# Performance work log

Hardware: AMD Instinct MI355X
Metric: run time of the kernel (lower is better)

The kernel has to match this reference:

```python
import jax, jax.numpy as jnp
import numpy as np

N_NODES = 100000
N_EDGES = 1600000
HIDDEN = 512
LOWER = 128
NUM_RELS = 6


def setup_inputs() -> dict:
    key = jax.random.key(0)
    ks = jax.random.split(key, 16)
    glorot = lambda k, shape: jax.random.normal(k, shape, jnp.float32) * (2.0 / (shape[-2] + shape[-1])) ** 0.5
    return {
        "h_origin": jax.random.normal(ks[0], (N_NODES, HIDDEN), jnp.float32),
        "edge_src": jax.random.randint(ks[1], (N_EDGES,), 0, N_NODES, jnp.int32),
        "edge_dst": jax.random.randint(ks[2], (N_EDGES,), 0, N_NODES, jnp.int32),
        "edge_type": jax.random.randint(ks[3], (N_EDGES,), 0, NUM_RELS, jnp.int32),
        "W_lower": glorot(ks[4], (HIDDEN, LOWER)),
        "b_lower": jnp.zeros((LOWER,), jnp.float32),
        "W1": glorot(ks[5], (NUM_RELS, LOWER, LOWER)),
        "b1": jnp.zeros((LOWER,), jnp.float32),
        "W2": glorot(ks[6], (NUM_RELS, LOWER, LOWER)),
        "b2": jnp.zeros((LOWER,), jnp.float32),
        "W3": glorot(ks[7], (NUM_RELS, LOWER, LOWER)),
        "b3": jnp.zeros((LOWER,), jnp.float32),
        "W_upper": glorot(ks[8], (LOWER, HIDDEN)),
        "b_upper": jnp.zeros((HIDDEN,), jnp.float32),
        "W_skip": glorot(ks[9], (HIDDEN, HIDDEN)),
        "b_skip": jnp.zeros((HIDDEN,), jnp.float32),
    }


def _ngcn_layer(h, W, b, edge_src, edge_dst, edge_type, n_nodes):
    # R-GCN layer: msg_e = h[src_e] @ W[rel_e]; h'_v = relu(sum_{e->v} msg_e + b)
    # Equivalent grouped form: transform all nodes by all relations (dense GEMMs),
    # then gather per-edge by (rel, src) -- same math as per-edge bmm.
    t = jnp.einsum("nd,rde->rne", h, W)          # [R, N, out]
    msg = t[edge_type, edge_src]                   # [E, out] gather
    agg = jax.ops.segment_sum(msg, edge_dst, num_segments=n_nodes)  # [N, out]
    return jax.nn.relu(agg + b)


def reference(h_origin, edge_src, edge_dst, edge_type,
              W_lower, b_lower, W1, b1, W2, b2, W3, b3,
              W_upper, b_upper, W_skip, b_skip):
    n_nodes = h_origin.shape[0]
    # lower: Linear + ReLU (hidden -> lower)
    h = jax.nn.relu(h_origin @ W_lower + b_lower)
    # three NGCN (R-GCN) layers, num_rels = 6
    h = _ngcn_layer(h, W1, b1, edge_src, edge_dst, edge_type, n_nodes)
    h = _ngcn_layer(h, W2, b2, edge_src, edge_dst, edge_type, n_nodes)
    h = _ngcn_layer(h, W3, b3, edge_src, edge_dst, edge_type, n_nodes)
    # upper(h) + skipper(origin): bg.ndata['h'] = upper(h) + skipper(origin_ndata)
    out = jax.nn.relu(h @ W_upper + b_upper) + jax.nn.relu(h_origin @ W_skip + b_skip)
    return out
```

## Files before the change

kernel.cpp:

```cpp
#include <hip/hip_runtime.h>
#include <hip/hip_bf16.h>

#define NN 100000
#define NE 1600000
#define HID 512
#define LOW 128
#define NR  6
#define NBINS (NN * NR)

typedef short  bf16x8 __attribute__((ext_vector_type(8)));
typedef float  f32x4  __attribute__((ext_vector_type(4)));

__device__ __forceinline__ unsigned short f2bf(float x) {
    __hip_bfloat16 h = __float2bfloat16(x);
    return __builtin_bit_cast(unsigned short, h);
}
__device__ __forceinline__ float bf2f(unsigned short u) {
    return __builtin_bit_cast(float, (unsigned int)u << 16);
}

__device__ __forceinline__ void stage_tile(const unsigned short* __restrict__ G,
                                           int r0, int k0, int Kstride, int Rmax,
                                           char* lds_base, int tid)
{
    #pragma unroll
    for (int is = 0; is < 4; ++is) {
        int L   = is * 4096 + tid * 16;
        int row = L >> 7;
        int c   = ((L >> 4) & 7) ^ (row & 7);
        int gr  = r0 + row;
        gr = (gr < Rmax) ? gr : (Rmax - 1);
        const char* src = (const char*)G + ((size_t)gr * Kstride + k0) * 2 + c * 16;
        __builtin_amdgcn_global_load_lds(
            (const __attribute__((address_space(1))) void*)src,
            (__attribute__((address_space(3))) void*)(lds_base + is * 4096 + (tid & 192) * 16),
            16, 0, 0);
    }
}

__device__ __forceinline__ bf16x8 lds_frag(const char* lds_base, int row, int clog)
{
    return *(const bf16x8*)(lds_base + row * 128 + ((clog ^ (row & 7)) << 4));
}

__global__ __launch_bounds__(256, 2)
void gemm_bf16(const unsigned short* __restrict__ A,
               const unsigned short* __restrict__ Bt,
               const float* __restrict__ bias,
               unsigned short* __restrict__ C,
               int M, int N, int K)
{
    __shared__ __align__(16) char lA[16384];
    __shared__ __align__(16) char lB[16384];

    const int tid  = threadIdx.x;
    const int lane = tid & 63;
    const int wid  = tid >> 6;
    const int wm   = wid >> 1;
    const int wn   = wid & 1;
    const int m0   = blockIdx.y * 128;
    const int n0   = blockIdx.x * 128;

    f32x4 acc[4][4] = {};

    for (int k0 = 0; k0 < K; k0 += 64) {
        stage_tile(A,  m0, k0, K, M, lA, tid);
        stage_tile(Bt, n0, k0, K, N, lB, tid);
        __syncthreads();
        #pragma unroll
        for (int kk = 0; kk < 2; ++kk) {
            const int clog = kk * 4 + (lane >> 4);
            bf16x8 af[4], bfr[4];
            #pragma unroll
            for (int i = 0; i < 4; ++i)
                af[i] = lds_frag(lA, wm * 64 + i * 16 + (lane & 15), clog);
            #pragma unroll
            for (int j = 0; j < 4; ++j)
                bfr[j] = lds_frag(lB, wn * 64 + j * 16 + (lane & 15), clog);
            #pragma unroll
            for (int i = 0; i < 4; ++i)
                #pragma unroll
                for (int j = 0; j < 4; ++j)
                    acc[i][j] = __builtin_amdgcn_mfma_f32_16x16x32_bf16(
                        af[i], bfr[j], acc[i][j], 0, 0, 0);
        }
        __syncthreads();
    }

    const int col_l = lane & 15;
    const int rgrp  = lane >> 4;
    #pragma unroll
    for (int i = 0; i < 4; ++i) {
        #pragma unroll
        for (int j = 0; j < 4; ++j) {
            int col  = n0 + wn * 64 + j * 16 + col_l;
            float bv = bias[col];
            #pragma unroll
            for (int r = 0; r < 4; ++r) {
                int row = m0 + wm * 64 + i * 16 + rgrp * 4 + r;
                if (row < M)
                    C[(size_t)row * N + col] = f2bf(fmaxf(acc[i][j][r] + bv, 0.f));
            }
        }
    }
}

__global__ __launch_bounds__(256, 2)
void gemm_out_fused(const unsigned short* __restrict__ h,
                    const unsigned short* __restrict__ Wut,
                    const float* __restrict__ bu,
                    const unsigned short* __restrict__ hob,
                    const unsigned short* __restrict__ Wst,
                    const float* __restrict__ bs,
                    float* __restrict__ out, int M)
{
    __shared__ __align__(16) char lA[16384];
    __shared__ __align__(16) char lB[16384];

    const int tid  = threadIdx.x;
    const int lane = tid & 63;
    const int wid  = tid >> 6;
    const int wm   = wid >> 1;
    const int wn   = wid & 1;

    const int nwg  = gridDim.x;
    const int cpx  = nwg >> 3;
    const int idx  = (blockIdx.x & 7) * cpx + (blockIdx.x >> 3);
    const int m0   = (idx >> 2) * 128;
    const int n0   = (idx & 3) * 128;

    f32x4 acc1[4][4] = {};
    f32x4 acc2[4][4] = {};

    for (int k0 = 0; k0 < LOW; k0 += 64) {
        stage_tile(h,   m0, k0, LOW, M,   lA, tid);
        stage_tile(Wut, n0, k0, LOW, HID, lB, tid);
        __syncthreads();
        #pragma unroll
        for (int kk = 0; kk < 2; ++kk) {
            const int clog = kk * 4 + (lane >> 4);
            bf16x8 af[4], bfr[4];
            #pragma unroll
            for (int i = 0; i < 4; ++i)
                af[i] = lds_frag(lA, wm * 64 + i * 16 + (lane & 15), clog);
            #pragma unroll
            for (int j = 0; j < 4; ++j)
                bfr[j] = lds_frag(lB, wn * 64 + j * 16 + (lane & 15), clog);
            #pragma unroll
            for (int i = 0; i < 4; ++i)
                #pragma unroll
                for (int j = 0; j < 4; ++j)
                    acc1[i][j] = __builtin_amdgcn_mfma_f32_16x16x32_bf16(
                        af[i], bfr[j], acc1[i][j], 0, 0, 0);
        }
        __syncthreads();
    }
    for (int k0 = 0; k0 < HID; k0 += 64) {
        stage_tile(hob, m0, k0, HID, M,   lA, tid);
        stage_tile(Wst, n0, k0, HID, HID, lB, tid);
        __syncthreads();
        #pragma unroll
        for (int kk = 0; kk < 2; ++kk) {
            const int clog = kk * 4 + (lane >> 4);
            bf16x8 af[4], bfr[4];
            #pragma unroll
            for (int i = 0; i < 4; ++i)
                af[i] = lds_frag(lA, wm * 64 + i * 16 + (lane & 15), clog);
            #pragma unroll
            for (int j = 0; j < 4; ++j)
                bfr[j] = lds_frag(lB, wn * 64 + j * 16 + (lane & 15), clog);
            #pragma unroll
            for (int i = 0; i < 4; ++i)
                #pragma unroll
                for (int j = 0; j < 4; ++j)
                    acc2[i][j] = __builtin_amdgcn_mfma_f32_16x16x32_bf16(
                        af[i], bfr[j], acc2[i][j], 0, 0, 0);
        }
        __syncthreads();
    }

    const int col_l = lane & 15;
    const int rgrp  = lane >> 4;
    #pragma unroll
    for (int i = 0; i < 4; ++i) {
        #pragma unroll
        for (int j = 0; j < 4; ++j) {
            int col   = n0 + wn * 64 + j * 16 + col_l;
            float bv1 = bu[col], bv2 = bs[col];
            #pragma unroll
            for (int r = 0; r < 4; ++r) {
                int row = m0 + wm * 64 + i * 16 + rgrp * 4 + r;
                if (row < M)
                    out[(size_t)row * HID + col] =
                        fmaxf(acc1[i][j][r] + bv1, 0.f) + fmaxf(acc2[i][j][r] + bv2, 0.f);
            }
        }
    }
}

__global__ __launch_bounds__(256)
void conv_f32_bf16(const float4* __restrict__ in, ushort4* __restrict__ out, int n4)
{
    for (int i = blockIdx.x * 256 + threadIdx.x; i < n4; i += gridDim.x * 256) {
        float4 v = in[i];
        ushort4 o;
        o.x = f2bf(v.x); o.y = f2bf(v.y); o.z = f2bf(v.z); o.w = f2bf(v.w);
        out[i] = o;
    }
}

__global__ __launch_bounds__(256)
void transpose_all(const float* __restrict__ Wl_, const float* __restrict__ W1,
                   const float* __restrict__ W2, const float* __restrict__ W3,
                   const float* __restrict__ Wu, const float* __restrict__ Ws_,
                   unsigned short* __restrict__ wlt, unsigned short* __restrict__ w1t,
                   unsigned short* __restrict__ w2t, unsigned short* __restrict__ w3t,
                   unsigned short* __restrict__ wut, unsigned short* __restrict__ wst)
{
    int idx = blockIdx.x * 256 + threadIdx.x;
    const float* W;
    unsigned short* T;
    int R, local, cshift;
    if (idx < 65536)       { W = Wl_; T = wlt; R = 512; local = idx;          cshift = 7; }
    else if (idx < 163840) { W = W1;  T = w1t; R = 768; local = idx - 65536;  cshift = 7; }
    else if (idx < 262144) { W = W2;  T = w2t; R = 768; local = idx - 163840; cshift = 7; }
    else if (idx < 360448) { W = W3;  T = w3t; R = 768; local = idx - 262144; cshift = 7; }
    else if (idx < 425984) { W = Wu;  T = wut; R = 128; local = idx - 360448; cshift = 9; }
    else                   { W = Ws_; T = wst; R = 512; local = idx - 425984; cshift = 9; }
    int r = local >> cshift;
    int c = local & ((1 << cshift) - 1);
    T[(size_t)c * R + r] = f2bf(W[local]);
}

#define SCAN_VT 8
#define SCAN_BS 256
#define SCAN_CHUNK (SCAN_VT * SCAN_BS)
#define SCAN_NB ((NBINS + SCAN_CHUNK - 1) / SCAN_CHUNK)

__global__ __launch_bounds__(256)
void k_hist(const int* __restrict__ dst, const int* __restrict__ typ,
            int* __restrict__ deg, int E)
{
    int e = blockIdx.x * 256 + threadIdx.x;
    if (e < E) atomicAdd(&deg[dst[e] * NR + typ[e]], 1);
}

__global__ __launch_bounds__(SCAN_BS)
void k_scan_part(const int* __restrict__ deg, int* __restrict__ blocksum, int n)
{
    __shared__ int ps[SCAN_BS];
    const int t = threadIdx.x;
    const int lo = blockIdx.x * SCAN_CHUNK + t * SCAN_VT;
    int s = 0;
    #pragma unroll
    for (int k = 0; k < SCAN_VT; ++k) {
        int i = lo + k;
        if (i < n) s += deg[i];
    }
    ps[t] = s;
    __syncthreads();
    for (int off = SCAN_BS / 2; off > 0; off >>= 1) {
        if (t < off) ps[t] += ps[t + off];
        __syncthreads();
    }
    if (t == 0) blocksum[blockIdx.x] = ps[0];
}

__global__ __launch_bounds__(64)
void k_scan_mid(const int* __restrict__ blocksum, int* __restrict__ blockoff,
                int* __restrict__ rowstart, int nb, int n)
{
    if (threadIdx.x == 0) {
        int run = 0;
        for (int i = 0; i < nb; ++i) { blockoff[i] = run; run += blocksum[i]; }
        rowstart[n] = run;
    }
}

__global__ __launch_bounds__(SCAN_BS)
void k_scan_final(const int* __restrict__ deg, const int* __restrict__ blockoff,
                  int* __restrict__ rowstart, int* __restrict__ cursor, int n)
{
    __shared__ int ps[SCAN_BS];
    const int t = threadIdx.x;
    const int lo = blockIdx.x * SCAN_CHUNK + t * SCAN_VT;
    int local[SCAN_VT];
    int s = 0;
    #pragma unroll
    for (int k = 0; k < SCAN_VT; ++k) {
        int i = lo + k;
        int v = (i < n) ? deg[i] : 0;
        local[k] = v;
        s += v;
    }
    ps[t] = s;
    __syncthreads();
    for (int off = 1; off < SCAN_BS; off <<= 1) {
        int v = (t >= off) ? ps[t - off] : 0;
        __syncthreads();
        ps[t] += v;
        __syncthreads();
    }
    int run = blockoff[blockIdx.x] + ((t > 0) ? ps[t - 1] : 0);
    #pragma unroll
    for (int k = 0; k < SCAN_VT; ++k) {
        int i = lo + k;
        if (i < n) {
            rowstart[i] = run;
            cursor[i]   = run;
            run += local[k];
        }
    }
}

__global__ __launch_bounds__(256)
void k_fill(const int* __restrict__ src, const int* __restrict__ dst,
            const int* __restrict__ typ, int* __restrict__ cursor,
            int* __restrict__ list, int E)
{
    int e = blockIdx.x * 256 + threadIdx.x;
    if (e < E) {
        int pos = atomicAdd(&cursor[dst[e] * NR + typ[e]], 1);
        list[pos] = src[e];
    }
}

__global__ __launch_bounds__(256)
void gather_agg(const unsigned short* __restrict__ h,
                const int* __restrict__ rowstart,
                const int* __restrict__ list,
                unsigned short* __restrict__ S)
{
    const int v = (blockIdx.x * 256 + threadIdx.x) >> 5;
    if (v >= NN) return;
    const int lane = threadIdx.x & 31;
    const ushort4* hp = (const ushort4*)h;

    const int b0 = rowstart[v * NR + 0];
    const int b1 = rowstart[v * NR + 1];
    const int b2 = rowstart[v * NR + 2];
    const int b3 = rowstart[v * NR + 3];
    const int b4 = rowstart[v * NR + 4];
    const int b5 = rowstart[v * NR + 5];
    const int b6 = rowstart[v * NR + 6];
    const int n0 = b1 - b0, n1 = b2 - b1, n2 = b3 - b2;
    const int n3 = b4 - b3, n4 = b5 - b4, n5 = b6 - b5;
    const int kmax = max(max(max(n0, n1), max(n2, n3)), max(n4, n5));

    float a0x=0.f,a0y=0.f,a0z=0.f,a0w=0.f, a1x=0.f,a1y=0.f,a1z=0.f,a1w=0.f;
    float a2x=0.f,a2y=0.f,a2z=0.f,a2w=0.f, a3x=0.f,a3y=0.f,a3z=0.f,a3w=0.f;
    float a4x=0.f,a4y=0.f,a4z=0.f,a4w=0.f, a5x=0.f,a5y=0.f,a5z=0.f,a5w=0.f;

    for (int k = 0; k < kmax; ++k) {
        int i0 = (k < n0) ? (b0 + k) : 0;
        int i1 = (k < n1) ? (b1 + k) : 0;
        int i2 = (k < n2) ? (b2 + k) : 0;
        int i3 = (k < n3) ? (b3 + k) : 0;
        int i4 = (k < n4) ? (b4 + k) : 0;
        int i5 = (k < n5) ? (b5 + k) : 0;
        int s0 = list[i0], s1 = list[i1], s2 = list[i2];
        int s3 = list[i3], s4 = list[i4], s5 = list[i5];
        ushort4 u0 = hp[(size_t)s0 * 32 + lane];
        ushort4 u1 = hp[(size_t)s1 * 32 + lane];
        ushort4 u2 = hp[(size_t)s2 * 32 + lane];
        ushort4 u3 = hp[(size_t)s3 * 32 + lane];
        ushort4 u4 = hp[(size_t)s4 * 32 + lane];
        ushort4 u5 = hp[(size_t)s5 * 32 + lane];
        if (k < n0) { a0x += bf2f(u0.x); a0y += bf2f(u0.y); a0z += bf2f(u0.z); a0w += bf2f(u0.w); }
        if (k < n1) { a1x += bf2f(u1.x); a1y += bf2f(u1.y); a1z += bf2f(u1.z); a1w += bf2f(u1.w); }
        if (k < n2) { a2x += bf2f(u2.x); a2y += bf2f(u2.y); a2z += bf2f(u2.z); a2w += bf2f(u2.w); }
        if (k < n3) { a3x += bf2f(u3.x); a3y += bf2f(u3.y); a3z += bf2f(u3.z); a3w += bf2f(u3.w); }
        if (k < n4) { a4x += bf2f(u4.x); a4y += bf2f(u4.y); a4z += bf2f(u4.z); a4w += bf2f(u4.w); }
        if (k < n5) { a5x += bf2f(u5.x); a5y += bf2f(u5.y); a5z += bf2f(u5.z); a5w += bf2f(u5.w); }
    }

    ushort4* o = (ushort4*)(S + (size_t)v * (NR * LOW));
    ushort4 w;
    w.x=f2bf(a0x); w.y=f2bf(a0y); w.z=f2bf(a0z); w.w=f2bf(a0w); o[0*32+lane]=w;
    w.x=f2bf(a1x); w.y=f2bf(a1y); w.z=f2bf(a1z); w.w=f2bf(a1w); o[1*32+lane]=w;
    w.x=f2bf(a2x); w.y=f2bf(a2y); w.z=f2bf(a2z); w.w=f2bf(a2w); o[2*32+lane]=w;
    w.x=f2bf(a3x); w.y=f2bf(a3y); w.z=f2bf(a3z); w.w=f2bf(a3w); o[3*32+lane]=w;
    w.x=f2bf(a4x); w.y=f2bf(a4y); w.z=f2bf(a4z); w.w=f2bf(a4w); o[4*32+lane]=w;
    w.x=f2bf(a5x); w.y=f2bf(a5y); w.z=f2bf(a5z); w.w=f2bf(a5w); o[5*32+lane]=w;
}

extern "C" void kernel_launch(void* const* d_in, const int* in_sizes, int n_in,
                              void* d_out, int out_size, void* d_ws, size_t ws_size,
                              hipStream_t stream)
{
    (void)in_sizes; (void)n_in; (void)out_size; (void)ws_size;

    const float* h_origin = (const float*)d_in[0];
    const int*   esrc     = (const int*)d_in[1];
    const int*   edst     = (const int*)d_in[2];
    const int*   etyp     = (const int*)d_in[3];
    const float* W_lower  = (const float*)d_in[4];
    const float* b_lower  = (const float*)d_in[5];
    const float* Wl[3]    = {(const float*)d_in[6], (const float*)d_in[8], (const float*)d_in[10]};
    const float* bl[3]    = {(const float*)d_in[7], (const float*)d_in[9], (const float*)d_in[11]};
    const float* W_upper  = (const float*)d_in[12];
    const float* b_upper  = (const float*)d_in[13];
    const float* W_skip   = (const float*)d_in[14];
    const float* b_skip   = (const float*)d_in[15];
    float*       out      = (float*)d_out;

    unsigned short* hob = (unsigned short*)d_ws;
    unsigned short* h   = hob + (size_t)NN * HID;
    unsigned short* S   = h + (size_t)NN * LOW;
    unsigned short* wlt = S + (size_t)NN * NR * LOW;
    unsigned short* w1t = wlt + (size_t)LOW * HID;
    unsigned short* w2t = w1t + (size_t)LOW * NR * LOW;
    unsigned short* w3t = w2t + (size_t)LOW * NR * LOW;
    unsigned short* wut = w3t + (size_t)LOW * NR * LOW;
    unsigned short* wst = wut + (size_t)HID * LOW;
    int* deg      = (int*)(wst + (size_t)HID * HID);
    int* rowstart = deg + NBINS;
    int* cursor   = rowstart + NBINS + 1;
    int* list     = cursor + NBINS;
    int* blocksum = list + NE;
    int* blockoff = blocksum + SCAN_NB;
    unsigned short* wtL[3] = {w1t, w2t, w3t};

    const unsigned eBlocks = (unsigned)((NE + 255) / 256);
    const unsigned mBlocks = (unsigned)((NN + 127) / 128);

    conv_f32_bf16<<<dim3(2048), dim3(256), 0, stream>>>(
        (const float4*)h_origin, (ushort4*)hob, NN * HID / 4);
    transpose_all<<<dim3(2688), dim3(256), 0, stream>>>(
        W_lower, Wl[0], Wl[1], Wl[2], W_upper, W_skip,
        wlt, w1t, w2t, w3t, wut, wst);

    hipMemsetAsync(deg, 0, NBINS * sizeof(int), stream);
    k_hist<<<dim3(eBlocks), dim3(256), 0, stream>>>(edst, etyp, deg, NE);
    k_scan_part<<<dim3(SCAN_NB), dim3(SCAN_BS), 0, stream>>>(deg, blocksum, NBINS);
    k_scan_mid<<<dim3(1), dim3(64), 0, stream>>>(blocksum, blockoff, rowstart, SCAN_NB, NBINS);
    k_scan_final<<<dim3(SCAN_NB), dim3(SCAN_BS), 0, stream>>>(deg, blockoff, rowstart, cursor, NBINS);
    k_fill<<<dim3(eBlocks), dim3(256), 0, stream>>>(esrc, edst, etyp, cursor, list, NE);

    gemm_bf16<<<dim3(1, mBlocks), dim3(256), 0, stream>>>(
        hob, wlt, b_lower, h, NN, LOW, HID);

    const unsigned gBlocks = (unsigned)(((size_t)NN * 32 + 255) / 256);
    for (int L = 0; L < 3; ++L) {
        gather_agg<<<dim3(gBlocks), dim3(256), 0, stream>>>(h, rowstart, list, S);
        gemm_bf16<<<dim3(1, mBlocks), dim3(256), 0, stream>>>(
            S, wtL[L], bl[L], h, NN, LOW, NR * LOW);
    }

    gemm_out_fused<<<dim3((HID / 128) * mBlocks), dim3(256), 0, stream>>>(
        h, wut, b_upper, hob, wst, b_skip, out, NN);
}
```

Baseline: 813.0 us.

## Split skip GEMM into separate 256-tile kernel and enlarge row tiles

The skip projection (h_origin @ W_skip) is moved out of the fused output kernel into its own GEMM with 256x256 tiles and 512 threads, writing a bf16 intermediate that the upper GEMM reads back in its epilogue. The lower and per-layer GEMMs switch to 256-row tiles with 512 threads, so each block stages the full 128-column weight slice once per 256 rows. The aim is better weight reuse and more MFMA work per LDS load. The cost is an extra bf16 write and read of a 100000x512 buffer, plus bf16 rounding of the skip term before the add.

```diff
diff --git a/kernel.cpp b/kernel.cpp
--- a/kernel.cpp
+++ b/kernel.cpp
@@ -38,19 +38,57 @@
     }
 }
 
+__device__ __forceinline__ void stage256_512(const unsigned short* __restrict__ G,
+                                             int r0, int k0, int Kstride, int Rmax,
+                                             char* lds_base, int tid)
+{
+    #pragma unroll
+    for (int is = 0; is < 4; ++is) {
+        int L   = is * 8192 + tid * 16;
+        int row = L >> 7;
+        int c   = ((L >> 4) & 7) ^ (row & 7);
+        int gr  = r0 + row;
+        gr = (gr < Rmax) ? gr : (Rmax - 1);
+        const char* src = (const char*)G + ((size_t)gr * Kstride + k0) * 2 + c * 16;
+        __builtin_amdgcn_global_load_lds(
+            (const __attribute__((address_space(1))) void*)src,
+            (__attribute__((address_space(3))) void*)(lds_base + is * 8192 + (tid >> 6) * 1024),
+            16, 0, 0);
+    }
+}
+
+__device__ __forceinline__ void stage128_512(const unsigned short* __restrict__ G,
+                                             int r0, int k0, int Kstride, int Rmax,
+                                             char* lds_base, int tid)
+{
+    #pragma unroll
+    for (int is = 0; is < 2; ++is) {
+        int L   = is * 8192 + tid * 16;
+        int row = L >> 7;
+        int c   = ((L >> 4) & 7) ^ (row & 7);
+        int gr  = r0 + row;
+        gr = (gr < Rmax) ? gr : (Rmax - 1);
+        const char* src = (const char*)G + ((size_t)gr * Kstride + k0) * 2 + c * 16;
+        __builtin_amdgcn_global_load_lds(
+            (const __attribute__((address_space(1))) void*)src,
+            (__attribute__((address_space(3))) void*)(lds_base + is * 8192 + (tid >> 6) * 1024),
+            16, 0, 0);
+    }
+}
+
 __device__ __forceinline__ bf16x8 lds_frag(const char* lds_base, int row, int clog)
 {
     return *(const bf16x8*)(lds_base + row * 128 + ((clog ^ (row & 7)) << 4));
 }
 
-__global__ __launch_bounds__(256, 2)
-void gemm_bf16(const unsigned short* __restrict__ A,
-               const unsigned short* __restrict__ Bt,
-               const float* __restrict__ bias,
-               unsigned short* __restrict__ C,
-               int M, int N, int K)
-{
-    __shared__ __align__(16) char lA[16384];
+__global__ __launch_bounds__(512, 4)
+void gemm_bm256(const unsigned short* __restrict__ A,
+                const unsigned short* __restrict__ Bt,
+                const float* __restrict__ bias,
+                unsigned short* __restrict__ C,
+                int M, int K)
+{
+    __shared__ __align__(16) char lA[32768];
     __shared__ __align__(16) char lB[16384];
 
     const int tid  = threadIdx.x;
@@ -58,14 +96,13 @@
     const int wid  = tid >> 6;
     const int wm   = wid >> 1;
     const int wn   = wid & 1;
-    const int m0   = blockIdx.y * 128;
-    const int n0   = blockIdx.x * 128;
+    const int m0   = blockIdx.x * 256;
 
     f32x4 acc[4][4] = {};
 
     for (int k0 = 0; k0 < K; k0 += 64) {
-        stage_tile(A,  m0, k0, K, M, lA, tid);
-        stage_tile(Bt, n0, k0, K, N, lB, tid);
+        stage256_512(A,  m0, k0, K, M,   lA, tid);
+        stage128_512(Bt, 0,  k0, K, LOW, lB, tid);
         __syncthreads();
         #pragma unroll
         for (int kk = 0; kk < 2; ++kk) {
@@ -93,25 +130,84 @@
     for (int i = 0; i < 4; ++i) {
         #pragma unroll
         for (int j = 0; j < 4; ++j) {
-            int col  = n0 + wn * 64 + j * 16 + col_l;
+            int col  = wn * 64 + j * 16 + col_l;
             float bv = bias[col];
             #pragma unroll
             for (int r = 0; r < 4; ++r) {
                 int row = m0 + wm * 64 + i * 16 + rgrp * 4 + r;
                 if (row < M)
-                    C[(size_t)row * N + col] = f2bf(fmaxf(acc[i][j][r] + bv, 0.f));
+                    C[(size_t)row * LOW + col] = f2bf(fmaxf(acc[i][j][r] + bv, 0.f));
             }
         }
     }
 }
 
+__global__ __launch_bounds__(512, 2)
+void gemm_skip256(const unsigned short* __restrict__ hob,
+                  const unsigned short* __restrict__ wst,
+                  const float* __restrict__ bs,
+                  unsigned short* __restrict__ skipb, int M)
+{
+    __shared__ __align__(16) char lA[32768];
+    __shared__ __align__(16) char lB[32768];
+
+    const int tid  = threadIdx.x;
+    const int lane = tid & 63;
+    const int wid  = tid >> 6;
+    const int wm   = wid >> 2;
+    const int wn   = wid & 3;
+    const int m0   = (blockIdx.x >> 1) * 256;
+    const int n0   = (blockIdx.x & 1) * 256;
+
+    f32x4 acc[8][4] = {};
+
+    for (int k0 = 0; k0 < HID; k0 += 64) {
+        stage256_512(hob, m0, k0, HID, M,   lA, tid);
+        stage256_512(wst, n0, k0, HID, HID, lB, tid);
+        __syncthreads();
+        #pragma unroll
+        for (int kk = 0; kk < 2; ++kk) {
+            const int clog = kk * 4 + (lane >> 4);
+            bf16x8 af[8], bfr[4];
+            #pragma unroll
+            for (int i = 0; i < 8; ++i)
+                af[i] = lds_frag(lA, wm * 128 + i * 16 + (lane & 15), clog);
+            #pragma unroll
+            for (int j = 0; j < 4; ++j)
+                bfr[j] = lds_frag(lB, wn * 64 + j * 16 + (lane & 15), clog);
+            #pragma unroll
+            for (int i = 0; i < 8; ++i)
+                #pragma unroll
+                for (int j = 0; j < 4; ++j)
+                    acc[i][j] = __builtin_amdgcn_mfma_f32_16x16x32_bf16(
+                        af[i], bfr[j], acc[i][j], 0, 0, 0);
+        }
+        __syncthreads();
+    }
+
+    const int col_l = lane & 15;
+    const int rgrp  = lane >> 4;
+    #pragma unroll
+    for (int i = 0; i < 8; ++i) {
+        #pragma unroll
+        for (int j = 0; j < 4; ++j) {
+            int col  = n0 + wn * 64 + j * 16 + col_l;
+            float bv = bs[col];
+            #pragma unroll
+            for (int r = 0; r < 4; ++r) {
+                int row = m0 + wm * 128 + i * 16 + rgrp * 4 + r;
+                if (row < M)
+                    skipb[(size_t)row * HID + col] = f2bf(fmaxf(acc[i][j][r] + bv, 0.f));
+            }
+        }
+    }
+}
+
 __global__ __launch_bounds__(256, 2)
-void gemm_out_fused(const unsigned short* __restrict__ h,
+void gemm_out_upper(const unsigned short* __restrict__ h,
                     const unsigned short* __restrict__ Wut,
                     const float* __restrict__ bu,
-                    const unsigned short* __restrict__ hob,
-                    const unsigned short* __restrict__ Wst,
-                    const float* __restrict__ bs,
+                    const unsigned short* __restrict__ skipb,
                     float* __restrict__ out, int M)
 {
     __shared__ __align__(16) char lA[16384];
@@ -129,8 +225,7 @@
     const int m0   = (idx >> 2) * 128;
     const int n0   = (idx & 3) * 128;
 
-    f32x4 acc1[4][4] = {};
-    f32x4 acc2[4][4] = {};
+    f32x4 acc[4][4] = {};
 
     for (int k0 = 0; k0 < LOW; k0 += 64) {
         stage_tile(h,   m0, k0, LOW, M,   lA, tid);
@@ -150,31 +245,8 @@
             for (int i = 0; i < 4; ++i)
                 #pragma unroll
                 for (int j = 0; j < 4; ++j)
-                    acc1[i][j] = __builtin_amdgcn_mfma_f32_16x16x32_bf16(
-                        af[i], bfr[j], acc1[i][j], 0, 0, 0);
-        }
-        __syncthreads();
-    }
-    for (int k0 = 0; k0 < HID; k0 += 64) {
-        stage_tile(hob, m0, k0, HID, M,   lA, tid);
-        stage_tile(Wst, n0, k0, HID, HID, lB, tid);
-        __syncthreads();
-        #pragma unroll
-        for (int kk = 0; kk < 2; ++kk) {
-            const int clog = kk * 4 + (lane >> 4);
-            bf16x8 af[4], bfr[4];
-            #pragma unroll
-            for (int i = 0; i < 4; ++i)
-                af[i] = lds_frag(lA, wm * 64 + i * 16 + (lane & 15), clog);
-            #pragma unroll
-            for (int j = 0; j < 4; ++j)
-                bfr[j] = lds_frag(lB, wn * 64 + j * 16 + (lane & 15), clog);
-            #pragma unroll
-            for (int i = 0; i < 4; ++i)
-                #pragma unroll
-                for (int j = 0; j < 4; ++j)
-                    acc2[i][j] = __builtin_amdgcn_mfma_f32_16x16x32_bf16(
-                        af[i], bfr[j], acc2[i][j], 0, 0, 0);
+                    acc[i][j] = __builtin_amdgcn_mfma_f32_16x16x32_bf16(
+                        af[i], bfr[j], acc[i][j], 0, 0, 0);
         }
         __syncthreads();
     }
@@ -185,14 +257,15 @@
     for (int i = 0; i < 4; ++i) {
         #pragma unroll
         for (int j = 0; j < 4; ++j) {
-            int col   = n0 + wn * 64 + j * 16 + col_l;
-            float bv1 = bu[col], bv2 = bs[col];
+            int col  = n0 + wn * 64 + j * 16 + col_l;
+            float bv = bu[col];
             #pragma unroll
             for (int r = 0; r < 4; ++r) {
                 int row = m0 + wm * 64 + i * 16 + rgrp * 4 + r;
-                if (row < M)
-                    out[(size_t)row * HID + col] =
-                        fmaxf(acc1[i][j][r] + bv1, 0.f) + fmaxf(acc2[i][j][r] + bv2, 0.f);
+                if (row < M) {
+                    float sk = bf2f(skipb[(size_t)row * HID + col]);
+                    out[(size_t)row * HID + col] = fmaxf(acc[i][j][r] + bv, 0.f) + sk;
+                }
             }
         }
     }
@@ -404,15 +477,16 @@
     const float* b_skip   = (const float*)d_in[15];
     float*       out      = (float*)d_out;
 
-    unsigned short* hob = (unsigned short*)d_ws;
-    unsigned short* h   = hob + (size_t)NN * HID;
-    unsigned short* S   = h + (size_t)NN * LOW;
-    unsigned short* wlt = S + (size_t)NN * NR * LOW;
-    unsigned short* w1t = wlt + (size_t)LOW * HID;
-    unsigned short* w2t = w1t + (size_t)LOW * NR * LOW;
-    unsigned short* w3t = w2t + (size_t)LOW * NR * LOW;
-    unsigned short* wut = w3t + (size_t)LOW * NR * LOW;
-    unsigned short* wst = wut + (size_t)HID * LOW;
+    unsigned short* hob   = (unsigned short*)d_ws;
+    unsigned short* h     = hob + (size_t)NN * HID;
+    unsigned short* S     = h + (size_t)NN * LOW;
+    unsigned short* skipb = S + (size_t)NN * NR * LOW;
+    unsigned short* wlt   = skipb + (size_t)NN * HID;
+    unsigned short* w1t   = wlt + (size_t)LOW * HID;
+    unsigned short* w2t   = w1t + (size_t)LOW * NR * LOW;
+    unsigned short* w3t   = w2t + (size_t)LOW * NR * LOW;
+    unsigned short* wut   = w3t + (size_t)LOW * NR * LOW;
+    unsigned short* wst   = wut + (size_t)HID * LOW;
     int* deg      = (int*)(wst + (size_t)HID * HID);
     int* rowstart = deg + NBINS;
     int* cursor   = rowstart + NBINS + 1;
@@ -421,8 +495,9 @@
     int* blockoff = blocksum + SCAN_NB;
     unsigned short* wtL[3] = {w1t, w2t, w3t};
 
-    const unsigned eBlocks = (unsigned)((NE + 255) / 256);
-    const unsigned mBlocks = (unsigned)((NN + 127) / 128);
+    const unsigned eBlocks   = (unsigned)((NE + 255) / 256);
+    const unsigned mBlocks   = (unsigned)((NN + 127) / 128);
+    const unsigned mBlocks2  = (unsigned)((NN + 255) / 256);
 
     conv_f32_bf16<<<dim3(2048), dim3(256), 0, stream>>>(
         (const float4*)h_origin, (ushort4*)hob, NN * HID / 4);
@@ -437,16 +512,19 @@
     k_scan_final<<<dim3(SCAN_NB), dim3(SCAN_BS), 0, stream>>>(deg, blockoff, rowstart, cursor, NBINS);
     k_fill<<<dim3(eBlocks), dim3(256), 0, stream>>>(esrc, edst, etyp, cursor, list, NE);
 
-    gemm_bf16<<<dim3(1, mBlocks), dim3(256), 0, stream>>>(
-        hob, wlt, b_lower, h, NN, LOW, HID);
+    gemm_bm256<<<dim3(mBlocks2), dim3(512), 0, stream>>>(
+        hob, wlt, b_lower, h, NN, HID);
+
+    gemm_skip256<<<dim3(mBlocks2 * 2), dim3(512), 0, stream>>>(
+        hob, wst, b_skip, skipb, NN);
 
     const unsigned gBlocks = (unsigned)(((size_t)NN * 32 + 255) / 256);
     for (int L = 0; L < 3; ++L) {
         gather_agg<<<dim3(gBlocks), dim3(256), 0, stream>>>(h, rowstart, list, S);
-        gemm_bf16<<<dim3(1, mBlocks), dim3(256), 0, stream>>>(
-            S, wtL[L], bl[L], h, NN, LOW, NR * LOW);
-    }
-
-    gemm_out_fused<<<dim3((HID / 128) * mBlocks), dim3(256), 0, stream>>>(
-        h, wut, b_upper, hob, wst, b_skip, out, NN);
-}
+        gemm_bm256<<<dim3(mBlocks2), dim3(512), 0, stream>>>(
+            S, wtL[L], bl[L], h, NN, NR * LOW);
+    }
+
+    gemm_out_upper<<<dim3((HID / 128) * mBlocks), dim3(256), 0, stream>>>(
+        h, wut, b_upper, skipb, out, NN);
+}
```

Result: slower. 949.2 us (+16.8%).
